# Optimization experiments

Measured on AMD Instinct MI355X. Metric: run time of the kernel, lower is better.

Reference implementation:

```python
import jax, jax.numpy as jnp
import numpy as np

B, N, F = 4, 1024, 128
HID, EMB = 64, 32  # node_transform hidden, node embedding dim


def setup_inputs() -> dict:
    key = jax.random.key(0)
    ks = jax.random.split(key, 12)
    s = lambda fan_in: 1.0 / np.sqrt(fan_in)
    x = jax.random.normal(ks[0], (B, N, F), dtype=jnp.float32)
    adj_matrix = jax.random.uniform(ks[1], (N, N), dtype=jnp.float32)
    # node_transform: Linear(F, 64) -> ReLU -> Linear(64, 32)
    W1 = jax.random.uniform(ks[2], (F, HID), minval=-s(F), maxval=s(F))
    b1 = jax.random.uniform(ks[3], (HID,), minval=-s(F), maxval=s(F))
    W2 = jax.random.uniform(ks[4], (HID, EMB), minval=-s(HID), maxval=s(HID))
    b2 = jax.random.uniform(ks[5], (EMB,), minval=-s(HID), maxval=s(HID))
    # edge_attention: Linear(64, 32) -> ReLU -> Linear(32, 1) -> Sigmoid
    Wa1 = jax.random.uniform(ks[6], (2 * EMB, 32), minval=-s(2 * EMB), maxval=s(2 * EMB))
    ba1 = jax.random.uniform(ks[7], (32,), minval=-s(2 * EMB), maxval=s(2 * EMB))
    Wa2 = jax.random.uniform(ks[8], (32, 1), minval=-s(32), maxval=s(32))
    ba2 = jax.random.uniform(ks[9], (1,), minval=-s(32), maxval=s(32))
    return {"x": x, "adj_matrix": adj_matrix, "W1": W1, "b1": b1, "W2": W2,
            "b2": b2, "Wa1": Wa1, "ba1": ba1, "Wa2": Wa2, "ba2": ba2}


def reference(x, adj_matrix, W1, b1, W2, b2, Wa1, ba1, Wa2, ba2):
    # node_transform: [B,N,F] -> [B,N,32]
    h = jax.nn.relu(x @ W1 + b1)
    e = h @ W2 + b2  # node embeddings [B,N,EMB]
    # edge attention on concat(e_i, e_j): the first Linear on the concat
    # decomposes exactly as e_i @ Wa1[:EMB] + e_j @ Wa1[EMB:] + ba1,
    # avoiding the [B,N,N,2*EMB] concat tensor.
    a_i = e @ Wa1[:EMB]   # [B,N,32]
    a_j = e @ Wa1[EMB:]   # [B,N,32]
    pre = jax.nn.relu(a_i[:, :, None, :] + a_j[:, None, :, :] + ba1)  # [B,N,N,32]
    att = jax.nn.sigmoid(jnp.squeeze(pre @ Wa2, -1) + ba2[0])  # [B,N,N]
    att = att * adj_matrix[None, :, :]
    attended = jnp.einsum('bij,bjd->bid', att, e)  # [B,N,EMB]
    return jnp.mean(attended, axis=1)  # [B,EMB]
```

## Files before the change

### kernel.cpp

```cpp
#include <hip/hip_runtime.h>

#define B   4
#define N   1024
#define F   128
#define HID 64
#define EMB 32
#define NIC 128
#define IC  (N/NIC)
#define JB  256
#define NCH (NIC*4)

__global__ __launch_bounds__(256) void k1_embed(
    const float* __restrict__ x,  const float* __restrict__ W1, const float* __restrict__ b1,
    const float* __restrict__ W2, const float* __restrict__ b2,
    const float* __restrict__ Wa1,
    float* __restrict__ e, float* __restrict__ ai, float* __restrict__ aj)
{
    __shared__ float sh_x[4][F];
    __shared__ float sh_h[4][HID];
    __shared__ float sh_e[4][EMB];
    const int tid  = threadIdx.x;
    const int w    = tid >> 6;
    const int lane = tid & 63;
    const int r    = blockIdx.x * 4 + w;

    sh_x[w][lane]      = x[(size_t)r * F + lane];
    sh_x[w][lane + 64] = x[(size_t)r * F + 64 + lane];
    __syncthreads();

    float acc = b1[lane];
    #pragma unroll 16
    for (int k = 0; k < F; ++k)
        acc = fmaf(sh_x[w][k], W1[k * HID + lane], acc);
    sh_h[w][lane] = fmaxf(acc, 0.f);
    __syncthreads();

    const int d = lane & 31;
    float ev = b2[d];
    #pragma unroll 16
    for (int k = 0; k < HID; ++k)
        ev = fmaf(sh_h[w][k], W2[k * EMB + d], ev);
    if (lane < EMB) {
        sh_e[w][d] = ev;
        e[(size_t)r * EMB + d] = ev;
    }
    __syncthreads();

    const float* Wp = Wa1 + (lane < 32 ? 0 : EMB * EMB);
    float av = 0.f;
    #pragma unroll 16
    for (int k = 0; k < EMB; ++k)
        av = fmaf(sh_e[w][k], Wp[k * EMB + d], av);
    if (lane < 32) ai[(size_t)r * EMB + d] = av;
    else           aj[(size_t)r * EMB + d] = av;
}

__global__ __launch_bounds__(256) void k2_att(
    const float* __restrict__ ai, const float* __restrict__ aj,
    const float* __restrict__ ba1, const float* __restrict__ Wa2,
    const float* __restrict__ ba2, const float* __restrict__ adj,
    const float* __restrict__ e, float* __restrict__ out_part)
{
    const int ic   = blockIdx.x;
    const int b    = blockIdx.y >> 2;
    const int jblk = blockIdx.y & 3;
    const int tid  = threadIdx.x;
    const int j    = jblk * JB + tid;
    const int i0   = ic * IC;

    __shared__ float4 sh_ai[IC][EMB / 4];
    if (tid < IC * (EMB / 4)) {
        const int row = tid >> 3, c4 = tid & 7;
        sh_ai[row][c4] =
            ((const float4*)(ai + ((size_t)b * N + i0 + row) * EMB))[c4];
    }

    float ajb[EMB];
    {
        const float4* ap = (const float4*)(aj + ((size_t)b * N + j) * EMB);
        const float4* bp = (const float4*)ba1;
        #pragma unroll
        for (int q = 0; q < EMB / 4; ++q) {
            const float4 a4 = ap[q], b4 = bp[q];
            ajb[4 * q + 0] = a4.x + b4.x;
            ajb[4 * q + 1] = a4.y + b4.y;
            ajb[4 * q + 2] = a4.z + b4.z;
            ajb[4 * q + 3] = a4.w + b4.w;
        }
    }
    float w2[EMB];
    #pragma unroll
    for (int d2 = 0; d2 < EMB; ++d2) w2[d2] = Wa2[d2];
    const float bb = ba2[0];

    float adjv[IC];
    {
        const float* adjp = adj + (size_t)i0 * N + j;
        #pragma unroll
        for (int i = 0; i < IC; ++i) adjv[i] = adjp[(size_t)i * N];
    }
    __syncthreads();

    float ssum = 0.f;
    #pragma unroll
    for (int i = 0; i < IC; ++i) {
        const float4* arow = sh_ai[i];
        float acc0 = bb, acc1 = 0.f, acc2 = 0.f, acc3 = 0.f;
        #pragma unroll
        for (int q = 0; q < EMB / 4; ++q) {
            const float4 a4 = arow[q];
            acc0 = fmaf(fmaxf(a4.x + ajb[4 * q + 0], 0.f), w2[4 * q + 0], acc0);
            acc1 = fmaf(fmaxf(a4.y + ajb[4 * q + 1], 0.f), w2[4 * q + 1], acc1);
            acc2 = fmaf(fmaxf(a4.z + ajb[4 * q + 2], 0.f), w2[4 * q + 2], acc2);
            acc3 = fmaf(fmaxf(a4.w + ajb[4 * q + 3], 0.f), w2[4 * q + 3], acc3);
        }
        const float dot = (acc0 + acc1) + (acc2 + acc3);
        const float sg  = __builtin_amdgcn_rcpf(1.f + __expf(-dot));
        ssum = fmaf(sg, adjv[i], ssum);
    }

    __shared__ float sh_s[JB];
    sh_s[tid] = ssum;
    __syncthreads();

    const int d = tid & 31, g = tid >> 5;
    const float* ep = e + ((size_t)b * N + jblk * JB + g * 32) * EMB + d;
    float pacc = 0.f;
    #pragma unroll
    for (int jj = 0; jj < 32; ++jj)
        pacc = fmaf(sh_s[g * 32 + jj], ep[(size_t)jj * EMB], pacc);

    __shared__ float sh_r[8][EMB];
    sh_r[g][d] = pacc;
    __syncthreads();
    if (tid < EMB) {
        float s = 0.f;
        #pragma unroll
        for (int t = 0; t < 8; ++t) s += sh_r[t][tid];
        out_part[((size_t)b * NCH + ic * 4 + jblk) * EMB + tid] = s;
    }
}

__global__ __launch_bounds__(256) void k3_out(
    const float* __restrict__ out_part, float* __restrict__ out)
{
    const int b   = blockIdx.x;
    const int tid = threadIdx.x;
    const int d = tid & 31, g = tid >> 5;
    float acc = 0.f;
    for (int c = g; c < NCH; c += 8)
        acc += out_part[((size_t)b * NCH + c) * EMB + d];
    __shared__ float sh[8][EMB];
    sh[g][d] = acc;
    __syncthreads();
    if (tid < EMB) {
        float s = 0.f;
        #pragma unroll
        for (int t = 0; t < 8; ++t) s += sh[t][tid];
        out[b * EMB + tid] = s * (1.0f / N);
    }
}

extern "C" void kernel_launch(void* const* d_in, const int* in_sizes, int n_in,
                              void* d_out, int out_size, void* d_ws, size_t ws_size,
                              hipStream_t stream) {
    const float* x    = (const float*)d_in[0];
    const float* adj  = (const float*)d_in[1];
    const float* W1   = (const float*)d_in[2];
    const float* b1   = (const float*)d_in[3];
    const float* W2   = (const float*)d_in[4];
    const float* b2   = (const float*)d_in[5];
    const float* Wa1  = (const float*)d_in[6];
    const float* ba1  = (const float*)d_in[7];
    const float* Wa2  = (const float*)d_in[8];
    const float* ba2  = (const float*)d_in[9];
    float* out = (float*)d_out;

    float* ws = (float*)d_ws;
    float* e        = ws;
    float* ai       = ws + 131072;
    float* aj       = ws + 262144;
    float* out_part = ws + 393216;

    k1_embed<<<(B * N) / 4, 256, 0, stream>>>(x, W1, b1, W2, b2, Wa1, e, ai, aj);
    k2_att<<<dim3(NIC, B * 4), 256, 0, stream>>>(ai, aj, ba1, Wa2, ba2, adj, e, out_part);
    k3_out<<<B, 256, 0, stream>>>(out_part, out);
}
```

Before: 45.65 us.

## Enlarge attention i-chunks with software-pipelined adj loads and vectorize final reduction

The attention kernel now uses 32 i-chunks of 32 rows instead of 128 chunks of 8. Each thread's aj/ba1/Wa2 register setup is reused over four times as many rows, and the adjacency loads are double-buffered in groups of four to overlap with compute. The embedding kernel splits its first matmul into two accumulators and gains occupancy hints. The final reduction is vectorized with float4. Larger chunks leave only 512 blocks, which may reduce parallelism and latency hiding on a GPU with many CUs.

New measurement: 41.09 us. 10.0% less time.

```diff
diff --git a/kernel.cpp b/kernel.cpp
--- a/kernel.cpp
+++ b/kernel.cpp
@@ -5,12 +5,12 @@
 #define F   128
 #define HID 64
 #define EMB 32
-#define NIC 128
-#define IC  (N/NIC)
+#define NIS 32
+#define IC2 (N/NIS)
 #define JB  256
-#define NCH (NIC*4)
-
-__global__ __launch_bounds__(256) void k1_embed(
+#define NCH (NIS*4)
+
+__global__ __launch_bounds__(256, 4) void k1_embed(
     const float* __restrict__ x,  const float* __restrict__ W1, const float* __restrict__ b1,
     const float* __restrict__ W2, const float* __restrict__ b2,
     const float* __restrict__ Wa1,
@@ -28,16 +28,18 @@
     sh_x[w][lane + 64] = x[(size_t)r * F + 64 + lane];
     __syncthreads();
 
-    float acc = b1[lane];
-    #pragma unroll 16
-    for (int k = 0; k < F; ++k)
-        acc = fmaf(sh_x[w][k], W1[k * HID + lane], acc);
-    sh_h[w][lane] = fmaxf(acc, 0.f);
+    float acc0 = b1[lane], acc1 = 0.f;
+    #pragma unroll 8
+    for (int k = 0; k < F; k += 2) {
+        acc0 = fmaf(sh_x[w][k],     W1[k * HID + lane],       acc0);
+        acc1 = fmaf(sh_x[w][k + 1], W1[(k + 1) * HID + lane], acc1);
+    }
+    sh_h[w][lane] = fmaxf(acc0 + acc1, 0.f);
     __syncthreads();
 
     const int d = lane & 31;
     float ev = b2[d];
-    #pragma unroll 16
+    #pragma unroll 8
     for (int k = 0; k < HID; ++k)
         ev = fmaf(sh_h[w][k], W2[k * EMB + d], ev);
     if (lane < EMB) {
@@ -48,14 +50,38 @@
 
     const float* Wp = Wa1 + (lane < 32 ? 0 : EMB * EMB);
     float av = 0.f;
-    #pragma unroll 16
+    #pragma unroll 8
     for (int k = 0; k < EMB; ++k)
         av = fmaf(sh_e[w][k], Wp[k * EMB + d], av);
     if (lane < 32) ai[(size_t)r * EMB + d] = av;
     else           aj[(size_t)r * EMB + d] = av;
 }
 
-__global__ __launch_bounds__(256) void k2_att(
+#define LOADCH(av, t)                                    \
+    av[0] = adjp[(size_t)((t) * 4 + 0) * N];             \
+    av[1] = adjp[(size_t)((t) * 4 + 1) * N];             \
+    av[2] = adjp[(size_t)((t) * 4 + 2) * N];             \
+    av[3] = adjp[(size_t)((t) * 4 + 3) * N];
+
+#define COMPCH(av, t) do {                                                     \
+    _Pragma("unroll")                                                          \
+    for (int u = 0; u < 4; ++u) {                                              \
+        const float4* arow = sh_ai[(t) * 4 + u];                               \
+        float c0 = bb, c1 = 0.f, c2 = 0.f, c3 = 0.f;                           \
+        _Pragma("unroll")                                                      \
+        for (int q = 0; q < 8; ++q) {                                          \
+            const float4 a4 = arow[q];                                         \
+            c0 = fmaf(fmaxf(a4.x + ajb[4 * q + 0], 0.f), w2[4 * q + 0], c0);   \
+            c1 = fmaf(fmaxf(a4.y + ajb[4 * q + 1], 0.f), w2[4 * q + 1], c1);   \
+            c2 = fmaf(fmaxf(a4.z + ajb[4 * q + 2], 0.f), w2[4 * q + 2], c2);   \
+            c3 = fmaf(fmaxf(a4.w + ajb[4 * q + 3], 0.f), w2[4 * q + 3], c3);   \
+        }                                                                      \
+        const float dt = (c0 + c1) + (c2 + c3);                                \
+        const float sg = __builtin_amdgcn_rcpf(1.f + __expf(-dt));             \
+        ssum = fmaf(sg, av[u], ssum);                                          \
+    } } while (0)
+
+__global__ __launch_bounds__(256, 4) void k2_att(
     const float* __restrict__ ai, const float* __restrict__ aj,
     const float* __restrict__ ba1, const float* __restrict__ Wa2,
     const float* __restrict__ ba2, const float* __restrict__ adj,
@@ -66,10 +92,10 @@
     const int jblk = blockIdx.y & 3;
     const int tid  = threadIdx.x;
     const int j    = jblk * JB + tid;
-    const int i0   = ic * IC;
-
-    __shared__ float4 sh_ai[IC][EMB / 4];
-    if (tid < IC * (EMB / 4)) {
+    const int i0   = ic * IC2;
+
+    __shared__ float4 sh_ai[IC2][EMB / 4];
+    {
         const int row = tid >> 3, c4 = tid & 7;
         sh_ai[row][c4] =
             ((const float4*)(ai + ((size_t)b * N + i0 + row) * EMB))[c4];
@@ -78,46 +104,33 @@
     float ajb[EMB];
     {
         const float4* ap = (const float4*)(aj + ((size_t)b * N + j) * EMB);
-        const float4* bp = (const float4*)ba1;
         #pragma unroll
         for (int q = 0; q < EMB / 4; ++q) {
-            const float4 a4 = ap[q], b4 = bp[q];
-            ajb[4 * q + 0] = a4.x + b4.x;
-            ajb[4 * q + 1] = a4.y + b4.y;
-            ajb[4 * q + 2] = a4.z + b4.z;
-            ajb[4 * q + 3] = a4.w + b4.w;
+            const float4 a4 = ap[q];
+            ajb[4 * q + 0] = a4.x + ba1[4 * q + 0];
+            ajb[4 * q + 1] = a4.y + ba1[4 * q + 1];
+            ajb[4 * q + 2] = a4.z + ba1[4 * q + 2];
+            ajb[4 * q + 3] = a4.w + ba1[4 * q + 3];
         }
     }
     float w2[EMB];
     #pragma unroll
     for (int d2 = 0; d2 < EMB; ++d2) w2[d2] = Wa2[d2];
     const float bb = ba2[0];
-
-    float adjv[IC];
-    {
-        const float* adjp = adj + (size_t)i0 * N + j;
-        #pragma unroll
-        for (int i = 0; i < IC; ++i) adjv[i] = adjp[(size_t)i * N];
-    }
     __syncthreads();
 
     float ssum = 0.f;
-    #pragma unroll
-    for (int i = 0; i < IC; ++i) {
-        const float4* arow = sh_ai[i];
-        float acc0 = bb, acc1 = 0.f, acc2 = 0.f, acc3 = 0.f;
-        #pragma unroll
-        for (int q = 0; q < EMB / 4; ++q) {
-            const float4 a4 = arow[q];
-            acc0 = fmaf(fmaxf(a4.x + ajb[4 * q + 0], 0.f), w2[4 * q + 0], acc0);
-            acc1 = fmaf(fmaxf(a4.y + ajb[4 * q + 1], 0.f), w2[4 * q + 1], acc1);
-            acc2 = fmaf(fmaxf(a4.z + ajb[4 * q + 2], 0.f), w2[4 * q + 2], acc2);
-            acc3 = fmaf(fmaxf(a4.w + ajb[4 * q + 3], 0.f), w2[4 * q + 3], acc3);
-        }
-        const float dot = (acc0 + acc1) + (acc2 + acc3);
-        const float sg  = __builtin_amdgcn_rcpf(1.f + __expf(-dot));
-        ssum = fmaf(sg, adjv[i], ssum);
-    }
+    const float* adjp = adj + (size_t)i0 * N + j;
+    float avA[4], avB[4];
+    LOADCH(avA, 0);
+    LOADCH(avB, 1); COMPCH(avA, 0);
+    LOADCH(avA, 2); COMPCH(avB, 1);
+    LOADCH(avB, 3); COMPCH(avA, 2);
+    LOADCH(avA, 4); COMPCH(avB, 3);
+    LOADCH(avB, 5); COMPCH(avA, 4);
+    LOADCH(avA, 6); COMPCH(avB, 5);
+    LOADCH(avB, 7); COMPCH(avA, 6);
+    COMPCH(avB, 7);
 
     __shared__ float sh_s[JB];
     sh_s[tid] = ssum;
@@ -146,18 +159,28 @@
 {
     const int b   = blockIdx.x;
     const int tid = threadIdx.x;
-    const int d = tid & 31, g = tid >> 5;
-    float acc = 0.f;
-    for (int c = g; c < NCH; c += 8)
-        acc += out_part[((size_t)b * NCH + c) * EMB + d];
-    __shared__ float sh[8][EMB];
-    sh[g][d] = acc;
-    __syncthreads();
-    if (tid < EMB) {
-        float s = 0.f;
-        #pragma unroll
-        for (int t = 0; t < 8; ++t) s += sh[t][tid];
-        out[b * EMB + tid] = s * (1.0f / N);
+    const int d4  = tid & 7;
+    const int g   = tid >> 3;
+    const float4* op = (const float4*)(out_part + (size_t)b * NCH * EMB);
+
+    float4 acc = make_float4(0.f, 0.f, 0.f, 0.f);
+    #pragma unroll
+    for (int t = 0; t < NCH / 32; ++t) {
+        const float4 v = op[(size_t)(g + 32 * t) * (EMB / 4) + d4];
+        acc.x += v.x; acc.y += v.y; acc.z += v.z; acc.w += v.w;
+    }
+    __shared__ float4 sh[32][8];
+    sh[g][d4] = acc;
+    __syncthreads();
+    if (tid < 8) {
+        float4 s = make_float4(0.f, 0.f, 0.f, 0.f);
+        for (int gg = 0; gg < 32; ++gg) {
+            const float4 v = sh[gg][tid];
+            s.x += v.x; s.y += v.y; s.z += v.z; s.w += v.w;
+        }
+        const float inv = 1.0f / N;
+        ((float4*)(out + b * EMB))[tid] =
+            make_float4(s.x * inv, s.y * inv, s.z * inv, s.w * inv);
     }
 }
 
@@ -183,6 +206,6 @@
     float* out_part = ws + 393216;
 
     k1_embed<<<(B * N) / 4, 256, 0, stream>>>(x, W1, b1, W2, b2, Wa1, e, ai, aj);
-    k2_att<<<dim3(NIC, B * 4), 256, 0, stream>>>(ai, aj, ba1, Wa2, ba2, adj, e, out_part);
+    k2_att<<<dim3(NIS, B * 4), 256, 0, stream>>>(ai, aj, ba1, Wa2, ba2, adj, e, out_part);
     k3_out<<<B, 256, 0, stream>>>(out_part, out);
 }
```
